# Kernel optimization log

Hardware: AMD Instinct MI355X
Metric: run time of the kernel (lower is better)

Reference implementation:

```python
import jax, jax.numpy as jnp
import numpy as np

L = 6        # num_coupling_layers
T_DIM = 64   # t_dim
HALF = T_DIM // 2
COND = 128   # cond_dim
HID = 1024   # hidden_dim
B = 32768


def setup_inputs() -> dict:
    key = jax.random.key(0)
    ks = jax.random.split(key, 8)
    s_in = 1.0 / np.sqrt(HALF + COND)
    s_h = 1.0 / np.sqrt(HID)
    T = jax.random.normal(ks[0], (B, T_DIM), dtype=jnp.float32)
    cond = jax.random.normal(ks[1], (B, COND), dtype=jnp.float32)
    W1 = jax.random.normal(ks[2], (L, HALF + COND, HID), dtype=jnp.float32) * s_in
    b1 = jnp.zeros((L, HID), dtype=jnp.float32)
    W2 = jax.random.normal(ks[3], (L, HID, HID), dtype=jnp.float32) * s_h
    b2 = jnp.zeros((L, HID), dtype=jnp.float32)
    W3 = jax.random.normal(ks[4], (L, HID, 2 * HALF), dtype=jnp.float32) * s_h
    b3 = jnp.zeros((L, 2 * HALF), dtype=jnp.float32)
    return {"T": T, "cond": cond, "W1": W1, "b1": b1, "W2": W2, "b2": b2, "W3": W3, "b3": b3}


def reference(T, cond, W1, b1, W2, b2, W3, b3):
    # Conditional normalizing flow: 6 affine coupling layers with alternating
    # contiguous half masks. Even layers transform the first half, odd the second.
    def mlp(h, i):
        x = jax.nn.relu(h @ W1[i] + b1[i])
        x = jax.nn.relu(x @ W2[i] + b2[i])
        return x @ W3[i] + b3[i]

    z = T
    log_det = jnp.zeros(T.shape[0], dtype=T.dtype)
    for i in range(L):
        if i % 2 == 0:
            masked, unmasked = z[:, :HALF], z[:, HALF:]
        else:
            masked, unmasked = z[:, HALF:], z[:, :HALF]
        params = mlp(jnp.concatenate([unmasked, cond], axis=1), i)
        s = jnp.tanh(params[:, :HALF])
        t_shift = params[:, HALF:]
        y_masked = masked * jnp.exp(s) + t_shift
        if i % 2 == 0:
            z = jnp.concatenate([y_masked, unmasked], axis=1)
        else:
            z = jnp.concatenate([unmasked, y_masked], axis=1)
        log_det = log_det + jnp.sum(s, axis=1)
    return z, log_det
```

## Files before the change

### kernel.cpp

```cpp
#include <hip/hip_runtime.h>
#include <hip/hip_fp16.h>
#include <stdint.h>

typedef _Float16 f16;
typedef _Float16 f16x8 __attribute__((ext_vector_type(8)));
typedef float f32x4 __attribute__((ext_vector_type(4)));

#define NB 32768
#define LAYERS 6
#define AK 160
#define HID 1024

__device__ __forceinline__ void async_copy16(const void* g, void* l) {
  __builtin_amdgcn_global_load_lds(
      (const __attribute__((address_space(1))) void*)g,
      (__attribute__((address_space(3))) void*)l, 16, 0, 0);
}

__global__ void prep_batch(const float* __restrict__ T, const float* __restrict__ cond,
                           float* __restrict__ z, float* __restrict__ ld,
                           f16* __restrict__ A)
{
  const int S1 = NB * 64;
  const int S2 = S1 + NB;
  const int S3 = S2 + NB * 32;
  const int S4 = S3 + NB * 128;
  for (int i = blockIdx.x * blockDim.x + threadIdx.x; i < S4;
       i += gridDim.x * blockDim.x) {
    if (i < S1) {
      z[i] = T[i];
    } else if (i < S2) {
      ld[i - S1] = 0.0f;
    } else if (i < S3) {
      int r = i - S2;
      int row = r >> 5, j = r & 31;
      A[(size_t)row * AK + j] = (f16)T[row * 64 + 32 + j];
    } else {
      int r = i - S3;
      int row = r >> 7, j = r & 127;
      A[(size_t)row * AK + 32 + j] = (f16)cond[r];
    }
  }
}

__global__ void prep_weights(const float* __restrict__ W1, const float* __restrict__ W2,
                             const float* __restrict__ W3,
                             f16* __restrict__ W1t, f16* __restrict__ W2t,
                             f16* __restrict__ W3t)
{
  const int N2 = 6 << 20;
  const int N1 = N2 + 6 * 1024 * 160;
  const int N3 = N1 + 6 * 64 * 1024;
  for (int i = blockIdx.x * blockDim.x + threadIdx.x; i < N3;
       i += gridDim.x * blockDim.x) {
    if (i < N2) {
      int l = i >> 20, r = i & 0xFFFFF, n = r >> 10, k = r & 1023;
      W2t[i] = (f16)W2[((size_t)l << 20) + ((size_t)k << 10) + n];
    } else if (i < N1) {
      int t = i - N2;
      int l = t / 163840, r = t % 163840, n = r / 160, k = r % 160;
      W1t[t] = (f16)W1[(size_t)l * 163840 + (size_t)k * 1024 + n];
    } else {
      int t = i - N1;
      int l = t >> 16, r = t & 0xFFFF, n = r >> 10, k = r & 1023;
      W3t[t] = (f16)W3[((size_t)l << 16) + ((size_t)k << 6) + n];
    }
  }
}

__global__ __launch_bounds__(256, 2)
void gemm12(const f16* __restrict__ A, const int K,
            const f16* __restrict__ Wt,
            const float* __restrict__ bias,
            f16* __restrict__ C)
{
  __shared__ __align__(16) f16 As[2][256 * 32];
  __shared__ __align__(16) f16 Bs[2][128 * 32];
  const int tid  = threadIdx.x;
  const int wave = tid >> 6;
  const int lane = tid & 63;
  const int c15  = lane & 15;
  const int quad = lane >> 4;
  const int wm = (wave & 1) * 128;
  const int wn = (wave >> 1) * 64;

  const int b = blockIdx.x;
  const int x = b & 7, i = b >> 3;
  const long rowStart = (long)(x * 16 + (i >> 3)) * 256;
  const long colStart = (long)(i & 7) * 128;

  const f16* Ab = A  + rowStart * K;
  const f16* Bb = Wt + colStart * K;

  const int ra  = tid >> 2;
  const int kca = (((tid & 3) ^ ((ra >> 1) & 3))) * 8;

  f32x4 acc[8][4] = {};
  const int nK = K >> 5;

  auto stage = [&](int kt, int sel) {
    const long ko = (long)kt * 32;
    f16* as = &As[sel][0];
    f16* bs = &Bs[sel][0];
#pragma unroll
    for (int q = 0; q < 4; ++q)
      async_copy16(Ab + (long)(q * 64 + ra) * K + ko + kca,
                   as + (q * 256 + wave * 64) * 8);
#pragma unroll
    for (int q = 0; q < 2; ++q)
      async_copy16(Bb + (long)(q * 64 + ra) * K + ko + kca,
                   bs + (q * 256 + wave * 64) * 8);
  };

  stage(0, 0);
  for (int kt = 0; kt < nK; ++kt) {
    __syncthreads();
    if (kt + 1 < nK) stage(kt + 1, (kt + 1) & 1);
    const f16* as = &As[kt & 1][0];
    const f16* bs = &Bs[kt & 1][0];

    f16x8 a[8], bf[4];
#pragma unroll
    for (int mi = 0; mi < 8; ++mi) {
      const int R = wm + mi * 16 + c15;
      a[mi] = *(const f16x8*)&as[R * 32 + ((quad ^ ((R >> 1) & 3)) << 3)];
    }
#pragma unroll
    for (int ni = 0; ni < 4; ++ni) {
      const int R = wn + ni * 16 + c15;
      bf[ni] = *(const f16x8*)&bs[R * 32 + ((quad ^ ((R >> 1) & 3)) << 3)];
    }
#pragma unroll
    for (int mi = 0; mi < 8; ++mi)
#pragma unroll
      for (int ni = 0; ni < 4; ++ni)
        acc[mi][ni] = __builtin_amdgcn_mfma_f32_16x16x32_f16(a[mi], bf[ni], acc[mi][ni], 0, 0, 0);
  }

#pragma unroll
  for (int ni = 0; ni < 4; ++ni) {
    const long gn = colStart + wn + ni * 16 + c15;
    const float bv = bias[gn];
#pragma unroll
    for (int mi = 0; mi < 8; ++mi) {
#pragma unroll
      for (int r = 0; r < 4; ++r) {
        const long gm = rowStart + wm + mi * 16 + quad * 4 + r;
        float v = acc[mi][ni][r] + bv;
        v = fmaxf(v, 0.0f);
        C[gm * HID + gn] = (f16)v;
      }
    }
  }
}

__global__ __launch_bounds__(256, 4)
void gemm3_coupling(const f16* __restrict__ X2, const f16* __restrict__ W3t,
                    const float* __restrict__ b3, float* __restrict__ z,
                    float* __restrict__ log_det, f16* __restrict__ Anext,
                    const int maskoff)
{
  __shared__ __align__(16) f16 As[2][128 * 32];
  __shared__ __align__(16) f16 Bs[2][64 * 32];
  const int tid = threadIdx.x;
  const int wave = tid >> 6, lane = tid & 63;
  const int c15 = lane & 15, quad = lane >> 4;
  const int wm = wave * 32;
  const long rowStart = (long)blockIdx.x * 128;

  const f16* Ab = X2 + rowStart * HID;
  const int ra  = tid >> 2;
  const int kca = (((tid & 3) ^ ((ra >> 1) & 3))) * 8;

  f32x4 acc[2][4] = {};

  auto stage = [&](int kt, int sel) {
    const long ko = (long)kt * 32;
    f16* as = &As[sel][0];
    f16* bs = &Bs[sel][0];
#pragma unroll
    for (int q = 0; q < 2; ++q)
      async_copy16(Ab + (long)(q * 64 + ra) * HID + ko + kca,
                   as + (q * 256 + wave * 64) * 8);
    async_copy16(W3t + (long)ra * HID + ko + kca,
                 bs + (wave * 64) * 8);
  };

  stage(0, 0);
  for (int kt = 0; kt < 32; ++kt) {
    __syncthreads();
    if (kt + 1 < 32) stage(kt + 1, (kt + 1) & 1);
    const f16* as = &As[kt & 1][0];
    const f16* bs = &Bs[kt & 1][0];

    f16x8 a[2], bf[4];
#pragma unroll
    for (int mi = 0; mi < 2; ++mi) {
      const int R = wm + mi * 16 + c15;
      a[mi] = *(const f16x8*)&as[R * 32 + ((quad ^ ((R >> 1) & 3)) << 3)];
    }
#pragma unroll
    for (int ni = 0; ni < 4; ++ni) {
      const int R = ni * 16 + c15;
      bf[ni] = *(const f16x8*)&bs[R * 32 + ((quad ^ ((R >> 1) & 3)) << 3)];
    }
#pragma unroll
    for (int mi = 0; mi < 2; ++mi)
#pragma unroll
      for (int ni = 0; ni < 4; ++ni)
        acc[mi][ni] = __builtin_amdgcn_mfma_f32_16x16x32_f16(a[mi], bf[ni], acc[mi][ni], 0, 0, 0);
  }

#pragma unroll
  for (int mi = 0; mi < 2; ++mi) {
    float sp[4] = {0.0f, 0.0f, 0.0f, 0.0f};
#pragma unroll
    for (int ni = 0; ni < 2; ++ni) {
      const int j = ni * 16 + c15;
      const float bs = b3[j];
      const float bt = b3[32 + j];
#pragma unroll
      for (int r = 0; r < 4; ++r) {
        const long gm = rowStart + wm + mi * 16 + quad * 4 + r;
        const float sv = acc[mi][ni][r] + bs;
        const float e2 = __expf(2.0f * sv);
        const float s  = 1.0f - 2.0f / (e2 + 1.0f);
        const float tv = acc[mi][ni + 2][r] + bt;
        const float m  = z[gm * 64 + maskoff + j];
        const float y  = fmaf(m, __expf(s), tv);
        z[gm * 64 + maskoff + j] = y;
        Anext[gm * AK + j] = (f16)y;
        sp[r] += s;
      }
    }
#pragma unroll
    for (int r = 0; r < 4; ++r) {
      float v = sp[r];
      v += __shfl_xor(v, 1);
      v += __shfl_xor(v, 2);
      v += __shfl_xor(v, 4);
      v += __shfl_xor(v, 8);
      if (c15 == 0) {
        const long gm = rowStart + wm + mi * 16 + quad * 4 + r;
        log_det[gm] += v;
      }
    }
  }
}

extern "C" void kernel_launch(void* const* d_in, const int* in_sizes, int n_in,
                              void* d_out, int out_size, void* d_ws, size_t ws_size,
                              hipStream_t stream) {
  (void)in_sizes; (void)n_in; (void)out_size; (void)ws_size;
  const float* T    = (const float*)d_in[0];
  const float* cond = (const float*)d_in[1];
  const float* W1   = (const float*)d_in[2];
  const float* b1   = (const float*)d_in[3];
  const float* W2   = (const float*)d_in[4];
  const float* b2   = (const float*)d_in[5];
  const float* W3   = (const float*)d_in[6];
  const float* b3   = (const float*)d_in[7];

  float* z  = (float*)d_out;
  float* ld = z + (size_t)NB * 64;

  f16* A   = (f16*)d_ws;
  f16* X1  = A   + (size_t)NB * AK;
  f16* X2  = X1  + (size_t)NB * HID;
  f16* W1t = X2  + (size_t)NB * HID;
  f16* W2t = W1t + (size_t)6 * 1024 * 160;
  f16* W3t = W2t + ((size_t)6 << 20);

  prep_batch<<<2048, 256, 0, stream>>>(T, cond, z, ld, A);
  prep_weights<<<2048, 256, 0, stream>>>(W1, W2, W3, W1t, W2t, W3t);

  const int g12 = (NB / 256) * (HID / 128);
  for (int l = 0; l < LAYERS; ++l) {
    gemm12<<<g12, 256, 0, stream>>>(A, AK, W1t + (size_t)l * 1024 * 160,
                                    b1 + l * 1024, X1);
    gemm12<<<g12, 256, 0, stream>>>(X1, HID, W2t + ((size_t)l << 20),
                                    b2 + l * 1024, X2);
    const int maskoff = (l & 1) ? 32 : 0;
    gemm3_coupling<<<NB / 128, 256, 0, stream>>>(X2, W3t + (size_t)l * 64 * 1024,
                                                 b3 + l * 64, z, ld, A, maskoff);
  }
}
```

Before: 910.2 us.

## Enlarge GEMM tile to 256x256 and switch to 32x32x16 MFMA

```diff
diff --git a/kernel.cpp b/kernel.cpp
--- a/kernel.cpp
+++ b/kernel.cpp
@@ -5,6 +5,7 @@
 typedef _Float16 f16;
 typedef _Float16 f16x8 __attribute__((ext_vector_type(8)));
 typedef float f32x4 __attribute__((ext_vector_type(4)));
+typedef float f32x16 __attribute__((ext_vector_type(16)));
 
 #define NB 32768
 #define LAYERS 6
@@ -68,26 +69,26 @@
   }
 }
 
-__global__ __launch_bounds__(256, 2)
+__global__ __launch_bounds__(256, 1)
 void gemm12(const f16* __restrict__ A, const int K,
             const f16* __restrict__ Wt,
             const float* __restrict__ bias,
             f16* __restrict__ C)
 {
   __shared__ __align__(16) f16 As[2][256 * 32];
-  __shared__ __align__(16) f16 Bs[2][128 * 32];
+  __shared__ __align__(16) f16 Bs[2][256 * 32];
   const int tid  = threadIdx.x;
   const int wave = tid >> 6;
   const int lane = tid & 63;
-  const int c15  = lane & 15;
-  const int quad = lane >> 4;
+  const int l31  = lane & 31;
+  const int half = lane >> 5;
   const int wm = (wave & 1) * 128;
-  const int wn = (wave >> 1) * 64;
+  const int wn = (wave >> 1) * 128;
 
   const int b = blockIdx.x;
   const int x = b & 7, i = b >> 3;
-  const long rowStart = (long)(x * 16 + (i >> 3)) * 256;
-  const long colStart = (long)(i & 7) * 128;
+  const long rowStart = (long)(x * 16 + (i >> 2)) * 256;
+  const long colStart = (long)(i & 3) * 256;
 
   const f16* Ab = A  + rowStart * K;
   const f16* Bb = Wt + colStart * K;
@@ -95,7 +96,7 @@
   const int ra  = tid >> 2;
   const int kca = (((tid & 3) ^ ((ra >> 1) & 3))) * 8;
 
-  f32x4 acc[8][4] = {};
+  f32x16 acc[4][4] = {};
   const int nK = K >> 5;
 
   auto stage = [&](int kt, int sel) {
@@ -107,7 +108,7 @@
       async_copy16(Ab + (long)(q * 64 + ra) * K + ko + kca,
                    as + (q * 256 + wave * 64) * 8);
 #pragma unroll
-    for (int q = 0; q < 2; ++q)
+    for (int q = 0; q < 4; ++q)
       async_copy16(Bb + (long)(q * 64 + ra) * K + ko + kca,
                    bs + (q * 256 + wave * 64) * 8);
   };
@@ -119,34 +120,42 @@
     const f16* as = &As[kt & 1][0];
     const f16* bs = &Bs[kt & 1][0];
 
-    f16x8 a[8], bf[4];
-#pragma unroll
-    for (int mi = 0; mi < 8; ++mi) {
-      const int R = wm + mi * 16 + c15;
-      a[mi] = *(const f16x8*)&as[R * 32 + ((quad ^ ((R >> 1) & 3)) << 3)];
+    f16x8 af[2][4], bf[2][4];
+#pragma unroll
+    for (int mi = 0; mi < 4; ++mi) {
+      const int R = wm + mi * 32 + l31;
+      const int sw = (R >> 1) & 3;
+      af[0][mi] = *(const f16x8*)&as[(R * 4 + (half ^ sw)) * 8];
+      af[1][mi] = *(const f16x8*)&as[(R * 4 + ((2 + half) ^ sw)) * 8];
     }
 #pragma unroll
     for (int ni = 0; ni < 4; ++ni) {
-      const int R = wn + ni * 16 + c15;
-      bf[ni] = *(const f16x8*)&bs[R * 32 + ((quad ^ ((R >> 1) & 3)) << 3)];
-    }
-#pragma unroll
-    for (int mi = 0; mi < 8; ++mi)
-#pragma unroll
-      for (int ni = 0; ni < 4; ++ni)
-        acc[mi][ni] = __builtin_amdgcn_mfma_f32_16x16x32_f16(a[mi], bf[ni], acc[mi][ni], 0, 0, 0);
+      const int R = wn + ni * 32 + l31;
+      const int sw = (R >> 1) & 3;
+      bf[0][ni] = *(const f16x8*)&bs[(R * 4 + (half ^ sw)) * 8];
+      bf[1][ni] = *(const f16x8*)&bs[(R * 4 + ((2 + half) ^ sw)) * 8];
+    }
+#pragma unroll
+    for (int ks = 0; ks < 2; ++ks)
+#pragma unroll
+      for (int mi = 0; mi < 4; ++mi)
+#pragma unroll
+        for (int ni = 0; ni < 4; ++ni)
+          acc[mi][ni] = __builtin_amdgcn_mfma_f32_32x32x16_f16(
+              af[ks][mi], bf[ks][ni], acc[mi][ni], 0, 0, 0);
   }
 
 #pragma unroll
   for (int ni = 0; ni < 4; ++ni) {
-    const long gn = colStart + wn + ni * 16 + c15;
+    const long gn = colStart + wn + ni * 32 + l31;
     const float bv = bias[gn];
 #pragma unroll
-    for (int mi = 0; mi < 8; ++mi) {
-#pragma unroll
-      for (int r = 0; r < 4; ++r) {
-        const long gm = rowStart + wm + mi * 16 + quad * 4 + r;
-        float v = acc[mi][ni][r] + bv;
+    for (int mi = 0; mi < 4; ++mi) {
+#pragma unroll
+      for (int reg = 0; reg < 16; ++reg) {
+        const int rowIn = (reg & 3) + 8 * (reg >> 2) + 4 * half;
+        const long gm = rowStart + wm + mi * 32 + rowIn;
+        float v = acc[mi][ni][reg] + bv;
         v = fmaxf(v, 0.0f);
         C[gm * HID + gn] = (f16)v;
       }
@@ -274,7 +283,7 @@
   prep_batch<<<2048, 256, 0, stream>>>(T, cond, z, ld, A);
   prep_weights<<<2048, 256, 0, stream>>>(W1, W2, W3, W1t, W2t, W3t);
 
-  const int g12 = (NB / 256) * (HID / 128);
+  const int g12 = (NB / 256) * (HID / 256);
   for (int l = 0; l < LAYERS; ++l) {
     gemm12<<<g12, 256, 0, stream>>>(A, AK, W1t + (size_t)l * 1024 * 160,
                                     b1 + l * 1024, X1);
```

New measurement: 1.068 ms. +17.3%, slower.

## Shrink gemm12 tile to 128x128 and use LDS-tiled weight transpose

Applied to the files above, without the earlier changes.

```diff
diff --git a/kernel.cpp b/kernel.cpp
--- a/kernel.cpp
+++ b/kernel.cpp
@@ -43,50 +43,50 @@
   }
 }
 
-__global__ void prep_weights(const float* __restrict__ W1, const float* __restrict__ W2,
-                             const float* __restrict__ W3,
-                             f16* __restrict__ W1t, f16* __restrict__ W2t,
-                             f16* __restrict__ W3t)
-{
-  const int N2 = 6 << 20;
-  const int N1 = N2 + 6 * 1024 * 160;
-  const int N3 = N1 + 6 * 64 * 1024;
-  for (int i = blockIdx.x * blockDim.x + threadIdx.x; i < N3;
-       i += gridDim.x * blockDim.x) {
-    if (i < N2) {
-      int l = i >> 20, r = i & 0xFFFFF, n = r >> 10, k = r & 1023;
-      W2t[i] = (f16)W2[((size_t)l << 20) + ((size_t)k << 10) + n];
-    } else if (i < N1) {
-      int t = i - N2;
-      int l = t / 163840, r = t % 163840, n = r / 160, k = r % 160;
-      W1t[t] = (f16)W1[(size_t)l * 163840 + (size_t)k * 1024 + n];
-    } else {
-      int t = i - N1;
-      int l = t >> 16, r = t & 0xFFFF, n = r >> 10, k = r & 1023;
-      W3t[t] = (f16)W3[((size_t)l << 16) + ((size_t)k << 6) + n];
-    }
-  }
-}
-
-__global__ __launch_bounds__(256, 2)
+__global__ void wtrans(const float* __restrict__ W, f16* __restrict__ Wt,
+                       const int K_, const int N_)
+{
+  __shared__ float t[64][65];
+  const long off = (long)blockIdx.z * K_ * N_;
+  const float* Wl = W + off;
+  f16* Wtl = Wt + off;
+  const int k0 = blockIdx.y * 64, n0 = blockIdx.x * 64;
+  const int tx = threadIdx.x & 63, ty4 = threadIdx.x >> 6;
+#pragma unroll
+  for (int r = ty4; r < 64; r += 4) {
+    const int k = k0 + r;
+    if (k < K_) t[r][tx] = Wl[(long)k * N_ + n0 + tx];
+  }
+  __syncthreads();
+  const int k = k0 + tx;
+  if (k < K_) {
+#pragma unroll
+    for (int r = ty4; r < 64; r += 4) {
+      const int n = n0 + r;
+      Wtl[(long)n * K_ + k] = (f16)t[tx][r];
+    }
+  }
+}
+
+__global__ __launch_bounds__(256, 3)
 void gemm12(const f16* __restrict__ A, const int K,
             const f16* __restrict__ Wt,
             const float* __restrict__ bias,
             f16* __restrict__ C)
 {
-  __shared__ __align__(16) f16 As[2][256 * 32];
+  __shared__ __align__(16) f16 As[2][128 * 32];
   __shared__ __align__(16) f16 Bs[2][128 * 32];
   const int tid  = threadIdx.x;
   const int wave = tid >> 6;
   const int lane = tid & 63;
   const int c15  = lane & 15;
   const int quad = lane >> 4;
-  const int wm = (wave & 1) * 128;
+  const int wm = (wave & 1) * 64;
   const int wn = (wave >> 1) * 64;
 
   const int b = blockIdx.x;
   const int x = b & 7, i = b >> 3;
-  const long rowStart = (long)(x * 16 + (i >> 3)) * 256;
+  const long rowStart = (long)(x * 32 + (i >> 3)) * 128;
   const long colStart = (long)(i & 7) * 128;
 
   const f16* Ab = A  + rowStart * K;
@@ -95,7 +95,7 @@
   const int ra  = tid >> 2;
   const int kca = (((tid & 3) ^ ((ra >> 1) & 3))) * 8;
 
-  f32x4 acc[8][4] = {};
+  f32x4 acc[4][4] = {};
   const int nK = K >> 5;
 
   auto stage = [&](int kt, int sel) {
@@ -103,7 +103,7 @@
     f16* as = &As[sel][0];
     f16* bs = &Bs[sel][0];
 #pragma unroll
-    for (int q = 0; q < 4; ++q)
+    for (int q = 0; q < 2; ++q)
       async_copy16(Ab + (long)(q * 64 + ra) * K + ko + kca,
                    as + (q * 256 + wave * 64) * 8);
 #pragma unroll
@@ -119,9 +119,9 @@
     const f16* as = &As[kt & 1][0];
     const f16* bs = &Bs[kt & 1][0];
 
-    f16x8 a[8], bf[4];
-#pragma unroll
-    for (int mi = 0; mi < 8; ++mi) {
+    f16x8 a[4], bf[4];
+#pragma unroll
+    for (int mi = 0; mi < 4; ++mi) {
       const int R = wm + mi * 16 + c15;
       a[mi] = *(const f16x8*)&as[R * 32 + ((quad ^ ((R >> 1) & 3)) << 3)];
     }
@@ -131,10 +131,11 @@
       bf[ni] = *(const f16x8*)&bs[R * 32 + ((quad ^ ((R >> 1) & 3)) << 3)];
     }
 #pragma unroll
-    for (int mi = 0; mi < 8; ++mi)
+    for (int mi = 0; mi < 4; ++mi)
 #pragma unroll
       for (int ni = 0; ni < 4; ++ni)
-        acc[mi][ni] = __builtin_amdgcn_mfma_f32_16x16x32_f16(a[mi], bf[ni], acc[mi][ni], 0, 0, 0);
+        acc[mi][ni] = __builtin_amdgcn_mfma_f32_16x16x32_f16(
+            a[mi], bf[ni], acc[mi][ni], 0, 0, 0);
   }
 
 #pragma unroll
@@ -142,7 +143,7 @@
     const long gn = colStart + wn + ni * 16 + c15;
     const float bv = bias[gn];
 #pragma unroll
-    for (int mi = 0; mi < 8; ++mi) {
+    for (int mi = 0; mi < 4; ++mi) {
 #pragma unroll
       for (int r = 0; r < 4; ++r) {
         const long gm = rowStart + wm + mi * 16 + quad * 4 + r;
@@ -272,11 +273,13 @@
   f16* W3t = W2t + ((size_t)6 << 20);
 
   prep_batch<<<2048, 256, 0, stream>>>(T, cond, z, ld, A);
-  prep_weights<<<2048, 256, 0, stream>>>(W1, W2, W3, W1t, W2t, W3t);
-
-  const int g12 = (NB / 256) * (HID / 128);
+  wtrans<<<dim3(16, 3, 6),  256, 0, stream>>>(W1, W1t, AK, 1024);
+  wtrans<<<dim3(16, 16, 6), 256, 0, stream>>>(W2, W2t, HID, 1024);
+  wtrans<<<dim3(1, 16, 6),  256, 0, stream>>>(W3, W3t, HID, 64);
+
+  const int g12 = (NB / 128) * (HID / 128);
   for (int l = 0; l < LAYERS; ++l) {
-    gemm12<<<g12, 256, 0, stream>>>(A, AK, W1t + (size_t)l * 1024 * 160,
+    gemm12<<<g12, 256, 0, stream>>>(A, AK, W1t + (size_t)l * 1024 * AK,
                                     b1 + l * 1024, X1);
     gemm12<<<g12, 256, 0, stream>>>(X1, HID, W2t + ((size_t)l << 20),
                                     b2 + l * 1024, X2);
```

Result: no change. 899.7 us (-1.1%).
